# Performance work log

Hardware: AMD Instinct MI355X
Metric: run time of the kernel (lower is better)

Reference implementation:

```python
import jax, jax.numpy as jnp
import numpy as np

MEM_DIM, H, W = 1024, 16, 16
HW = H * W
N_TOKENS, BATCH = 8192, 8
C1, C2, EPS = 0.01, 0.03, 1e-8


def setup_inputs() -> dict:
    key = jax.random.key(0)
    ks = jax.random.split(key, 5)
    std_w = 1.0 / np.sqrt(HW)
    return {
        "input_tokens": jax.random.normal(ks[0], (N_TOKENS, BATCH, HW), dtype=jnp.float32),
        "memory": jax.random.normal(ks[1], (MEM_DIM, H, W), dtype=jnp.float32) * 0.1,
        "Wq": jax.random.normal(ks[2], (HW, HW), dtype=jnp.float32) * std_w,
        "Wk": jax.random.normal(ks[3], (HW, HW), dtype=jnp.float32) * std_w,
        "Wv": jax.random.normal(ks[4], (HW, HW), dtype=jnp.float32) * std_w,
    }


def _ssim(q, k):
    # q: [N, HW], k: [M, HW] -> ssim: [N, M]
    qm = jnp.mean(q, axis=1, keepdims=True)          # [N,1]
    km = jnp.mean(k, axis=1, keepdims=True)          # [M,1]
    qv = jnp.var(q, axis=1, ddof=1, keepdims=True)   # torch.var unbiased
    kv = jnp.var(k, axis=1, ddof=1, keepdims=True)
    cov = ((q - qm) @ (k - km).T) / (HW - 1)         # [N,M]
    mean_prod = qm @ km.T                            # [N,M]
    numerator = (2.0 * mean_prod + C1) * (2.0 * cov + C2)
    denominator = (qm ** 2 + km.T ** 2 + C1) * (qv + kv.T + C2)
    return numerator / (denominator + EPS)


def reference(input_tokens, memory, Wq, Wk, Wv):
    Nt, B, F = input_tokens.shape
    x = input_tokens.reshape(Nt * B, HW)             # [N, HW]
    q = x @ Wq.T                                     # Linear(bias=False): x @ W^T
    m = memory.reshape(MEM_DIM, HW)
    k = m @ Wk.T
    v = m @ Wv.T
    ssim = _ssim(q, k)                               # [N, MEM_DIM]
    att = jax.nn.softmax(ssim, axis=1)
    out = (att @ v).reshape(Nt, B, F)
    return out
```

## Files before the change

kernel.cpp:

```cpp
#include <hip/hip_runtime.h>
#include <math.h>

typedef __attribute__((ext_vector_type(8)))  short bf16x8;
typedef __attribute__((ext_vector_type(16))) float f32x16;
typedef __attribute__((ext_vector_type(4)))  unsigned uint4v;

#define MFMA32(a, b, c) __builtin_amdgcn_mfma_f32_32x32x16_bf16((a), (b), (c), 0, 0, 0)

namespace {
constexpr int HWF   = 256;
constexpr int MEMD  = 1024;
constexpr int NROWS = 65536;
constexpr int TM    = 256;
constexpr int NT    = MEMD / 64;
constexpr int THREADS = 512;
constexpr float C1v  = 0.01f;
constexpr float C2v  = 0.03f;
constexpr float EPSv = 1e-8f;
constexpr float RK   = 1.0f / 255.0f;

constexpr int KB0 = 0;
constexpr int KB1 = 32768;
constexpr int VB0 = 65536;
constexpr int VB1 = 98304;
constexpr int SB0 = 131072;
constexpr int SB1 = 132096;
constexpr int LRED = 133120;
constexpr int SMEM_SZ = LRED + 1024;
}

__device__ __forceinline__ short f2bf(float f) {
    union { float f; unsigned u; } v; v.f = f;
    unsigned r = v.u + 0x7fffu + ((v.u >> 16) & 1u);
    return (short)(r >> 16);
}

__device__ __forceinline__ unsigned cvtpk(float a, float b) {
    unsigned r;
    asm("v_cvt_pk_bf16_f32 %0, %1, %2" : "=v"(r) : "v"(a), "v"(b));
    return r;
}

__device__ __forceinline__ void plswap(unsigned &a, unsigned &b) {
#if defined(__has_builtin) && __has_builtin(__builtin_amdgcn_permlane32_swap)
    auto r = __builtin_amdgcn_permlane32_swap((int)a, (int)b, false, false);
    a = (unsigned)r[0]; b = (unsigned)r[1];
#else
    const bool h = (threadIdx.x & 32) != 0;
    const unsigned ax = (unsigned)__shfl_xor((int)a, 32);
    const unsigned bx = (unsigned)__shfl_xor((int)b, 32);
    const unsigned na = h ? bx : a;
    const unsigned nb = h ? b : ax;
    a = na; b = nb;
#endif
}

__device__ __forceinline__ void dma_tile(const short* gbase, char* smem, int ldsbase,
                                         int wave, int lane) {
    const char* g = (const char*)gbase + wave * 4096 + lane * 16;
    char* l = smem + ldsbase + wave * 4096;
    #pragma unroll
    for (int i = 0; i < 4; ++i) {
        __builtin_amdgcn_global_load_lds(
            (const __attribute__((address_space(1))) unsigned int*)(g + i * 1024),
            (__attribute__((address_space(3))) unsigned int*)(l + i * 1024), 16, 0, 0);
    }
}

__device__ __forceinline__ void dma_stats(const float* sblob, char* smem, int sb,
                                          int jt, int lane) {
    __builtin_amdgcn_global_load_lds(
        (const __attribute__((address_space(1))) unsigned int*)
            ((const char*)sblob + (size_t)jt * 1024 + lane * 16),
        (__attribute__((address_space(3))) unsigned int*)(smem + sb + lane * 16), 16, 0, 0);
}

__global__ __launch_bounds__(256) void cast_wq(const float* __restrict__ W,
                                               short* __restrict__ Wb) {
    int i = blockIdx.x * 256 + threadIdx.x;
    Wb[i] = f2bf(W[i]);
}

__global__ __launch_bounds__(256) void prep_kv(
    const float* __restrict__ mem, const float* __restrict__ Wk,
    const float* __restrict__ Wv, short* __restrict__ kblob,
    short* __restrict__ vblob, float4* __restrict__ sblob)
{
    __shared__ __align__(16) float mrows[4][HWF];
    __shared__ float redS[4][8];
    const int t = threadIdx.x, j0 = blockIdx.x * 4;

    for (int r = 0; r < 4; ++r) mrows[r][t] = mem[(size_t)(j0 + r) * HWF + t];
    __syncthreads();

    const float4* wk4 = reinterpret_cast<const float4*>(Wk + (size_t)t * HWF);
    const float4* wv4 = reinterpret_cast<const float4*>(Wv + (size_t)t * HWF);
    float kt[4] = {0, 0, 0, 0}, vt[4] = {0, 0, 0, 0};
    for (int i = 0; i < 64; ++i) {
        const float4 a = wk4[i], b = wv4[i];
        for (int r = 0; r < 4; ++r) {
            const float4 m = reinterpret_cast<const float4*>(mrows[r])[i];
            kt[r] += m.x * a.x + m.y * a.y + m.z * a.z + m.w * a.w;
            vt[r] += m.x * b.x + m.y * b.y + m.z * b.z + m.w * b.w;
        }
    }

    const int wv_ = t >> 6, ln = t & 63;
    {
        float s[4];
        for (int r = 0; r < 4; ++r) s[r] = kt[r];
        for (int m = 1; m < 64; m <<= 1)
            for (int r = 0; r < 4; ++r) s[r] += __shfl_xor(s[r], m);
        if (ln == 0) {
            for (int r = 0; r < 4; ++r) redS[wv_][r] = s[r];
        }
    }
    __syncthreads();
    float kmv[4], kc4[4];
    for (int r = 0; r < 4; ++r) {
        kmv[r] = (redS[0][r] + redS[1][r] + redS[2][r] + redS[3][r]) * (1.f / HWF);
        kc4[r] = kt[r] - kmv[r];
    }
    {
        float s[4];
        for (int r = 0; r < 4; ++r) s[r] = kc4[r] * kc4[r];
        for (int m = 1; m < 64; m <<= 1)
            for (int r = 0; r < 4; ++r) s[r] += __shfl_xor(s[r], m);
        if (ln == 0) {
            for (int r = 0; r < 4; ++r) redS[wv_][4 + r] = s[r];
        }
    }
    __syncthreads();
    float kvv[4];
    for (int r = 0; r < 4; ++r)
        kvv[r] = (redS[0][4+r] + redS[1][4+r] + redS[2][4+r] + redS[3][4+r]) * (1.f / (HWF - 1));

    const int jt = j0 >> 6;
    for (int r = 0; r < 4; ++r) {
        const int ro = (j0 & 63) + r;
        kblob[jt * 16384 + ro * 256 + (((t >> 3) ^ (ro & 7)) * 8) + (t & 7)] = f2bf(kc4[r]);
        vblob[jt * 16384 + t * 64 + (((ro >> 3) ^ (t & 7)) * 8) + (ro & 7)] = f2bf(vt[r]);
    }
    if (t < 4) {
        sblob[j0 + t] = make_float4(2.f * kmv[t], kmv[t] * kmv[t] + C1v,
                                    kvv[t] + C2v, 0.f);
    }
}

__global__ __launch_bounds__(THREADS, 2) void attn(
    const float* __restrict__ x, const short* __restrict__ wq_bf,
    const short* __restrict__ kblob, const short* __restrict__ vblob,
    const float* __restrict__ sblob, float* __restrict__ out)
{
    __shared__ __align__(16) char smem[SMEM_SZ];
    const int t = threadIdx.x, wave = t >> 6, lane = t & 63;
    const int lo = lane & 31, hi = lane >> 5;
    const int rg = wave;
    const int n0 = blockIdx.x * TM;
    const int tok = n0 + 32 * rg + lo;

    dma_tile(kblob, smem, KB0, wave, lane);
    dma_tile(vblob, smem, VB0, wave, lane);
    if (wave == 0) dma_stats(sblob, smem, SB0, 0, lane);

    bf16x8 xB[16];
    {
        const float* xr = x + (size_t)tok * HWF;
        #pragma unroll
        for (int s = 0; s < 16; ++s) {
            const float4 a = *reinterpret_cast<const float4*>(xr + 16 * s + 8 * hi);
            const float4 b = *reinterpret_cast<const float4*>(xr + 16 * s + 8 * hi + 4);
            uint4v u;
            u[0] = cvtpk(a.x, a.y); u[1] = cvtpk(a.z, a.w);
            u[2] = cvtpk(b.x, b.y); u[3] = cvtpk(b.z, b.w);
            xB[s] = __builtin_bit_cast(bf16x8, u);
        }
    }

    f32x16 qD[8];
    #pragma unroll
    for (int nt = 0; nt < 8; ++nt) qD[nt] = (f32x16)(0.f);
    #pragma unroll
    for (int nt = 0; nt < 8; ++nt) {
        #pragma unroll
        for (int s = 0; s < 16; ++s) {
            const bf16x8 wa = *reinterpret_cast<const bf16x8*>(
                wq_bf + (size_t)(32 * nt + lo) * HWF + 16 * s + 8 * hi);
            qD[nt] = MFMA32(wa, xB[s], qD[nt]);
        }
    }

    float qs = 0.f, qss = 0.f;
    #pragma unroll
    for (int nt = 0; nt < 8; ++nt)
        #pragma unroll
        for (int i = 0; i < 16; ++i) {
            const float v = qD[nt][i];
            qs += v; qss = __builtin_fmaf(v, v, qss);
        }
    qs += __shfl_xor(qs, 32);
    qss += __shfl_xor(qss, 32);
    const float qm  = qs * (1.f / HWF);
    const float qv  = (qss - qs * qs * (1.f / HWF)) * (1.f / (HWF - 1));
    const float qm2 = qm * qm;

    bf16x8 qA[16];
    #pragma unroll
    for (int nt = 0; nt < 8; ++nt) {
        unsigned w[8];
        #pragma unroll
        for (int p = 0; p < 8; ++p) w[p] = cvtpk(qD[nt][2 * p], qD[nt][2 * p + 1]);
        #pragma unroll
        for (int h = 0; h < 2; ++h) {
            unsigned a0 = w[4 * h + 0], b0 = w[4 * h + 2];
            unsigned a1 = w[4 * h + 1], b1 = w[4 * h + 3];
            plswap(a0, b0); plswap(a1, b1);
            uint4v u; u[0] = a0; u[1] = a1; u[2] = b0; u[3] = b1;
            qA[2 * nt + h] = __builtin_bit_cast(bf16x8, u);
        }
    }

    f32x16 O4[8];
    #pragma unroll
    for (int ct = 0; ct < 8; ++ct) O4[ct] = (f32x16)(0.f);
    float l = 0.f;
    const int rx = (lo & 7);

    for (int jt = 0; jt < NT; ++jt) {
        const int cur = jt & 1;
        const int kb = cur ? KB1 : KB0, vb = cur ? VB1 : VB0, sb = cur ? SB1 : SB0;
        const int kbn = cur ? KB0 : KB1, vbn = cur ? VB0 : VB1, sbn = cur ? SB0 : SB1;
        __syncthreads();
        if (jt + 1 < NT) {
            dma_tile(kblob + (size_t)(jt + 1) * 16384, smem, kbn, wave, lane);
            dma_tile(vblob + (size_t)(jt + 1) * 16384, smem, vbn, wave, lane);
            if (wave == 0) dma_stats(sblob, smem, sbn, jt + 1, lane);
        }

        #pragma unroll
        for (int jh = 0; jh < 2; ++jh) {
            f32x16 sacc = (f32x16)(0.f);
            __builtin_amdgcn_s_setprio(1);
            #pragma unroll
            for (int s = 0; s < 16; ++s) {
                const bf16x8 kfr = *reinterpret_cast<const bf16x8*>(
                    smem + kb + jh * 16384 + lo * 512 + (((2 * s + hi) ^ rx) * 16));
                sacc = MFMA32(kfr, qA[s], sacc);
            }
            __builtin_amdgcn_s_setprio(0);

            unsigned pw[8];
            #pragma unroll
            for (int p = 0; p < 8; ++p) {
                float pr[2];
                #pragma unroll
                for (int q = 0; q < 2; ++q) {
                    const int i = 2 * p + q;
                    const float4 st = *reinterpret_cast<const float4*>(
                        smem + sb + hi * 64 + ((32 * jh + (i & 3) + 8 * (i >> 2)) * 16));
                    const float cov2 = __builtin_fmaf(sacc[i], 2.f * RK, C2v);
                    const float num  = __builtin_fmaf(st.x, qm, C1v) * cov2;
                    const float den  = __builtin_fmaf(qm2 + st.y, qv + st.z, EPSv);
                    pr[q] = __expf(__fdividef(num, den));
                    l += pr[q];
                }
                pw[p] = cvtpk(pr[0], pr[1]);
            }

            #pragma unroll
            for (int h = 0; h < 2; ++h) {
                const int ks = 2 * jh + h;
                unsigned a0 = pw[4 * h + 0], b0 = pw[4 * h + 2];
                unsigned a1 = pw[4 * h + 1], b1 = pw[4 * h + 3];
                plswap(a0, b0); plswap(a1, b1);
                uint4v u; u[0] = a0; u[1] = a1; u[2] = b0; u[3] = b1;
                const bf16x8 pa = __builtin_bit_cast(bf16x8, u);
                __builtin_amdgcn_s_setprio(1);
                #pragma unroll
                for (int ct = 0; ct < 8; ++ct) {
                    const bf16x8 vfr = *reinterpret_cast<const bf16x8*>(
                        smem + vb + (32 * ct + lo) * 128 + (((2 * ks + hi) ^ rx) * 16));
                    O4[ct] = MFMA32(pa, vfr, O4[ct]);
                }
                __builtin_amdgcn_s_setprio(0);
            }
        }
    }

    const float lf = l + __shfl_xor(l, 32);
    if (hi == 0)
        *reinterpret_cast<float*>(smem + LRED + (wave * 32 + lo) * 4) = lf;
    float rl[16];
    #pragma unroll
    for (int g = 0; g < 4; ++g) {
        const float4 lv = *reinterpret_cast<const float4*>(
            smem + LRED + wave * 128 + (8 * g + 4 * hi) * 4);
        rl[4 * g + 0] = 1.f / lv.x;
        rl[4 * g + 1] = 1.f / lv.y;
        rl[4 * g + 2] = 1.f / lv.z;
        rl[4 * g + 3] = 1.f / lv.w;
    }

    #pragma unroll
    for (int ct = 0; ct < 8; ++ct) {
        #pragma unroll
        for (int i = 0; i < 16; ++i) {
            const int row = 32 * rg + (i & 3) + 8 * (i >> 2) + 4 * hi;
            out[(size_t)(n0 + row) * HWF + 32 * ct + lo] = O4[ct][i] * rl[i];
        }
    }
}

extern "C" void kernel_launch(void* const* d_in, const int* in_sizes, int n_in,
                              void* d_out, int out_size, void* d_ws, size_t ws_size,
                              hipStream_t stream) {
    (void)in_sizes; (void)n_in; (void)out_size; (void)ws_size;
    const float* x   = (const float*)d_in[0];
    const float* mem = (const float*)d_in[1];
    const float* Wq  = (const float*)d_in[2];
    const float* Wk  = (const float*)d_in[3];
    const float* Wv  = (const float*)d_in[4];
    float* out = (float*)d_out;

    short* wq_bf = (short*)d_ws;
    short* kblob = wq_bf + 65536;
    short* vblob = kblob + (size_t)MEMD * HWF;
    float4* sblob = (float4*)(vblob + (size_t)MEMD * HWF);

    cast_wq<<<256, 256, 0, stream>>>(Wq, wq_bf);
    prep_kv<<<MEMD / 4, 256, 0, stream>>>(mem, Wk, Wv, kblob, vblob, sblob);
    attn<<<NROWS / TM, THREADS, 0, stream>>>(x, wq_bf, kblob, vblob,
                                             (const float*)sblob, out);
}
```

Measured before the change: 278.8 us.

## Shrink attention tiles to 128 tokens × 32 keys and preload SoA key stats once

The attention kernel moves from 256-token blocks of 8 waves with 64-key tiles to 128-token blocks of 4 waves with 32-key tiles. This halves LDS use (about 78KB instead of 134KB), so more blocks can be resident per CU. Key statistics are stored structure-of-arrays and loaded into LDS once at the start rather than streamed per tile, and the V blob swizzle is rewritten for the 32-key layout. The cost is twice as many loop iterations and barriers, plus less reuse of each K/V tile per block.

```diff
diff --git a/kernel.cpp b/kernel.cpp
--- a/kernel.cpp
+++ b/kernel.cpp
@@ -3,6 +3,7 @@
 
 typedef __attribute__((ext_vector_type(8)))  short bf16x8;
 typedef __attribute__((ext_vector_type(16))) float f32x16;
+typedef __attribute__((ext_vector_type(4)))  float f32x4;
 typedef __attribute__((ext_vector_type(4)))  unsigned uint4v;
 
 #define MFMA32(a, b, c) __builtin_amdgcn_mfma_f32_32x32x16_bf16((a), (b), (c), 0, 0, 0)
@@ -11,22 +12,21 @@
 constexpr int HWF   = 256;
 constexpr int MEMD  = 1024;
 constexpr int NROWS = 65536;
-constexpr int TM    = 256;
-constexpr int NT    = MEMD / 64;
-constexpr int THREADS = 512;
+constexpr int TM    = 128;
+constexpr int NT    = MEMD / 32;
+constexpr int THREADS = 256;
 constexpr float C1v  = 0.01f;
 constexpr float C2v  = 0.03f;
 constexpr float EPSv = 1e-8f;
 constexpr float RK   = 1.0f / 255.0f;
 
 constexpr int KB0 = 0;
-constexpr int KB1 = 32768;
-constexpr int VB0 = 65536;
-constexpr int VB1 = 98304;
-constexpr int SB0 = 131072;
-constexpr int SB1 = 132096;
-constexpr int LRED = 133120;
-constexpr int SMEM_SZ = LRED + 1024;
+constexpr int KB1 = 16384;
+constexpr int VB0 = 32768;
+constexpr int VB1 = 49152;
+constexpr int STATS = 65536;
+constexpr int LRED  = STATS + 12288;
+constexpr int SMEM_SZ = LRED + 512;
 }
 
 __device__ __forceinline__ short f2bf(float f) {
@@ -55,8 +55,8 @@
 #endif
 }
 
-__device__ __forceinline__ void dma_tile(const short* gbase, char* smem, int ldsbase,
-                                         int wave, int lane) {
+__device__ __forceinline__ void dma_tile16(const short* gbase, char* smem, int ldsbase,
+                                           int wave, int lane) {
     const char* g = (const char*)gbase + wave * 4096 + lane * 16;
     char* l = smem + ldsbase + wave * 4096;
     #pragma unroll
@@ -67,14 +67,6 @@
     }
 }
 
-__device__ __forceinline__ void dma_stats(const float* sblob, char* smem, int sb,
-                                          int jt, int lane) {
-    __builtin_amdgcn_global_load_lds(
-        (const __attribute__((address_space(1))) unsigned int*)
-            ((const char*)sblob + (size_t)jt * 1024 + lane * 16),
-        (__attribute__((address_space(3))) unsigned int*)(smem + sb + lane * 16), 16, 0, 0);
-}
-
 __global__ __launch_bounds__(256) void cast_wq(const float* __restrict__ W,
                                                short* __restrict__ Wb) {
     int i = blockIdx.x * 256 + threadIdx.x;
@@ -84,7 +76,7 @@
 __global__ __launch_bounds__(256) void prep_kv(
     const float* __restrict__ mem, const float* __restrict__ Wk,
     const float* __restrict__ Wv, short* __restrict__ kblob,
-    short* __restrict__ vblob, float4* __restrict__ sblob)
+    short* __restrict__ vblob, float* __restrict__ sblob)
 {
     __shared__ __align__(16) float mrows[4][HWF];
     __shared__ float redS[4][8];
@@ -135,15 +127,17 @@
     for (int r = 0; r < 4; ++r)
         kvv[r] = (redS[0][4+r] + redS[1][4+r] + redS[2][4+r] + redS[3][4+r]) * (1.f / (HWF - 1));
 
-    const int jt = j0 >> 6;
+    const int jt = j0 >> 5;
     for (int r = 0; r < 4; ++r) {
-        const int ro = (j0 & 63) + r;
-        kblob[jt * 16384 + ro * 256 + (((t >> 3) ^ (ro & 7)) * 8) + (t & 7)] = f2bf(kc4[r]);
-        vblob[jt * 16384 + t * 64 + (((ro >> 3) ^ (t & 7)) * 8) + (ro & 7)] = f2bf(vt[r]);
+        const int ro = (j0 & 31) + r;
+        kblob[jt * 8192 + ro * 256 + (((t >> 3) ^ (ro & 7)) * 8) + (t & 7)] = f2bf(kc4[r]);
+        vblob[jt * 8192 + t * 32 + (((ro >> 3) ^ (t & 3)) * 8) + (ro & 7)] = f2bf(vt[r]);
     }
     if (t < 4) {
-        sblob[j0 + t] = make_float4(2.f * kmv[t], kmv[t] * kmv[t] + C1v,
-                                    kvv[t] + C2v, 0.f);
+        const int j = j0 + t;
+        sblob[j]            = 2.f * kmv[t];
+        sblob[1024 + j]     = kmv[t] * kmv[t] + C1v;
+        sblob[2048 + j]     = kvv[t] + C2v;
     }
 }
 
@@ -159,9 +153,16 @@
     const int n0 = blockIdx.x * TM;
     const int tok = n0 + 32 * rg + lo;
 
-    dma_tile(kblob, smem, KB0, wave, lane);
-    dma_tile(vblob, smem, VB0, wave, lane);
-    if (wave == 0) dma_stats(sblob, smem, SB0, 0, lane);
+    dma_tile16(kblob, smem, KB0, wave, lane);
+    dma_tile16(vblob, smem, VB0, wave, lane);
+    #pragma unroll
+    for (int r = 0; r < 3; ++r) {
+        __builtin_amdgcn_global_load_lds(
+            (const __attribute__((address_space(1))) unsigned int*)
+                ((const char*)sblob + r * 4096 + wave * 1024 + lane * 16),
+            (__attribute__((address_space(3))) unsigned int*)
+                (smem + STATS + r * 4096 + wave * 1024 + lane * 16), 16, 0, 0);
+    }
 
     bf16x8 xB[16];
     {
@@ -228,62 +229,60 @@
 
     for (int jt = 0; jt < NT; ++jt) {
         const int cur = jt & 1;
-        const int kb = cur ? KB1 : KB0, vb = cur ? VB1 : VB0, sb = cur ? SB1 : SB0;
-        const int kbn = cur ? KB0 : KB1, vbn = cur ? VB0 : VB1, sbn = cur ? SB0 : SB1;
+        const int kb = cur ? KB1 : KB0, vb = cur ? VB1 : VB0;
+        const int kbn = cur ? KB0 : KB1, vbn = cur ? VB0 : VB1;
         __syncthreads();
         if (jt + 1 < NT) {
-            dma_tile(kblob + (size_t)(jt + 1) * 16384, smem, kbn, wave, lane);
-            dma_tile(vblob + (size_t)(jt + 1) * 16384, smem, vbn, wave, lane);
-            if (wave == 0) dma_stats(sblob, smem, sbn, jt + 1, lane);
-        }
-
-        #pragma unroll
-        for (int jh = 0; jh < 2; ++jh) {
-            f32x16 sacc = (f32x16)(0.f);
+            dma_tile16(kblob + (size_t)(jt + 1) * 8192, smem, kbn, wave, lane);
+            dma_tile16(vblob + (size_t)(jt + 1) * 8192, smem, vbn, wave, lane);
+        }
+
+        f32x16 sacc = (f32x16)(0.f);
+        __builtin_amdgcn_s_setprio(1);
+        #pragma unroll
+        for (int s = 0; s < 16; ++s) {
+            const bf16x8 kfr = *reinterpret_cast<const bf16x8*>(
+                smem + kb + lo * 512 + (((2 * s + hi) ^ rx) * 16));
+            sacc = MFMA32(kfr, qA[s], sacc);
+        }
+        __builtin_amdgcn_s_setprio(0);
+
+        unsigned pw[8];
+        #pragma unroll
+        for (int g = 0; g < 4; ++g) {
+            const int soff = (32 * jt + 8 * g + 4 * hi) * 4;
+            const f32x4 a4 = *reinterpret_cast<const f32x4*>(smem + STATS + soff);
+            const f32x4 b4 = *reinterpret_cast<const f32x4*>(smem + STATS + 4096 + soff);
+            const f32x4 c4 = *reinterpret_cast<const f32x4*>(smem + STATS + 8192 + soff);
+            float pr[4];
+            #pragma unroll
+            for (int q = 0; q < 4; ++q) {
+                const int i = 4 * g + q;
+                const float cov2 = __builtin_fmaf(sacc[i], 2.f * RK, C2v);
+                const float num  = __builtin_fmaf(a4[q], qm, C1v) * cov2;
+                const float den  = __builtin_fmaf(qm2 + b4[q], qv + c4[q], EPSv);
+                pr[q] = __expf(__fdividef(num, den));
+                l += pr[q];
+            }
+            pw[2 * g]     = cvtpk(pr[0], pr[1]);
+            pw[2 * g + 1] = cvtpk(pr[2], pr[3]);
+        }
+
+        #pragma unroll
+        for (int h = 0; h < 2; ++h) {
+            unsigned a0 = pw[4 * h + 0], b0 = pw[4 * h + 2];
+            unsigned a1 = pw[4 * h + 1], b1 = pw[4 * h + 3];
+            plswap(a0, b0); plswap(a1, b1);
+            uint4v u; u[0] = a0; u[1] = a1; u[2] = b0; u[3] = b1;
+            const bf16x8 pa = __builtin_bit_cast(bf16x8, u);
             __builtin_amdgcn_s_setprio(1);
             #pragma unroll
-            for (int s = 0; s < 16; ++s) {
-                const bf16x8 kfr = *reinterpret_cast<const bf16x8*>(
-                    smem + kb + jh * 16384 + lo * 512 + (((2 * s + hi) ^ rx) * 16));
-                sacc = MFMA32(kfr, qA[s], sacc);
+            for (int ct = 0; ct < 8; ++ct) {
+                const bf16x8 vfr = *reinterpret_cast<const bf16x8*>(
+                    smem + vb + (32 * ct + lo) * 64 + (((2 * h + hi) ^ (lo & 3)) * 16));
+                O4[ct] = MFMA32(pa, vfr, O4[ct]);
             }
             __builtin_amdgcn_s_setprio(0);
-
-            unsigned pw[8];
-            #pragma unroll
-            for (int p = 0; p < 8; ++p) {
-                float pr[2];
-                #pragma unroll
-                for (int q = 0; q < 2; ++q) {
-                    const int i = 2 * p + q;
-                    const float4 st = *reinterpret_cast<const float4*>(
-                        smem + sb + hi * 64 + ((32 * jh + (i & 3) + 8 * (i >> 2)) * 16));
-                    const float cov2 = __builtin_fmaf(sacc[i], 2.f * RK, C2v);
-                    const float num  = __builtin_fmaf(st.x, qm, C1v) * cov2;
-                    const float den  = __builtin_fmaf(qm2 + st.y, qv + st.z, EPSv);
-                    pr[q] = __expf(__fdividef(num, den));
-                    l += pr[q];
-                }
-                pw[p] = cvtpk(pr[0], pr[1]);
-            }
-
-            #pragma unroll
-            for (int h = 0; h < 2; ++h) {
-                const int ks = 2 * jh + h;
-                unsigned a0 = pw[4 * h + 0], b0 = pw[4 * h + 2];
-                unsigned a1 = pw[4 * h + 1], b1 = pw[4 * h + 3];
-                plswap(a0, b0); plswap(a1, b1);
-                uint4v u; u[0] = a0; u[1] = a1; u[2] = b0; u[3] = b1;
-                const bf16x8 pa = __builtin_bit_cast(bf16x8, u);
-                __builtin_amdgcn_s_setprio(1);
-                #pragma unroll
-                for (int ct = 0; ct < 8; ++ct) {
-                    const bf16x8 vfr = *reinterpret_cast<const bf16x8*>(
-                        smem + vb + (32 * ct + lo) * 128 + (((2 * ks + hi) ^ rx) * 16));
-                    O4[ct] = MFMA32(pa, vfr, O4[ct]);
-                }
-                __builtin_amdgcn_s_setprio(0);
-            }
         }
     }
 
@@ -293,12 +292,12 @@
     float rl[16];
     #pragma unroll
     for (int g = 0; g < 4; ++g) {
-        const float4 lv = *reinterpret_cast<const float4*>(
+        const f32x4 lv = *reinterpret_cast<const f32x4*>(
             smem + LRED + wave * 128 + (8 * g + 4 * hi) * 4);
-        rl[4 * g + 0] = 1.f / lv.x;
-        rl[4 * g + 1] = 1.f / lv.y;
-        rl[4 * g + 2] = 1.f / lv.z;
-        rl[4 * g + 3] = 1.f / lv.w;
+        rl[4 * g + 0] = 1.f / lv[0];
+        rl[4 * g + 1] = 1.f / lv[1];
+        rl[4 * g + 2] = 1.f / lv[2];
+        rl[4 * g + 3] = 1.f / lv[3];
     }
 
     #pragma unroll
@@ -325,10 +324,9 @@
     short* wq_bf = (short*)d_ws;
     short* kblob = wq_bf + 65536;
     short* vblob = kblob + (size_t)MEMD * HWF;
-    float4* sblob = (float4*)(vblob + (size_t)MEMD * HWF);
+    float* sblob = (float*)(vblob + (size_t)MEMD * HWF);
 
     cast_wq<<<256, 256, 0, stream>>>(Wq, wq_bf);
     prep_kv<<<MEMD / 4, 256, 0, stream>>>(mem, Wk, Wv, kblob, vblob, sblob);
-    attn<<<NROWS / TM, THREADS, 0, stream>>>(x, wq_bf, kblob, vblob,
-                                             (const float*)sblob, out);
-}
+    attn<<<NROWS / TM, THREADS, 0, stream>>>(x, wq_bf, kblob, vblob, sblob, out);
+}
```

Measured after the change: 259.1 us. 1.08x faster.
